# Optimization experiments

Measured on AMD Instinct MI355X. Metric: run time of the kernel, lower is better.

Reference implementation:

```python
import jax, jax.numpy as jnp
import numpy as np

N = 8388608  # batch size
RANGE = 0.02  # self.range in the original module


def setup_inputs() -> dict:
    key = jax.random.key(0)
    k1, k2 = jax.random.split(key)
    preds = jax.random.uniform(k1, (N, 3), dtype=jnp.float32)
    # target is binary ground truth (conditions compare against 0 and 1)
    target = jax.random.randint(k2, (N, 3), 0, 2).astype(jnp.float32)
    return {"preds": preds, "target": target}


def reference(preds, target):
    # Vectorized translation of the per-row scalar branching in RangeLoss.forward.
    p0, p1, p2 = preds[:, 0], preds[:, 1], preds[:, 2]
    t0, t1, t2 = target[:, 0], target[:, 1], target[:, 2]

    # columns 0 and 2: snap target to pred when pred is confidently correct
    t0 = jnp.where((p0 < 0.1) & (t0 == 0.0), p0, t0)
    t0 = jnp.where((p0 > 0.9) & (t0 == 1.0), p0, t0)
    t2 = jnp.where((p2 < 0.1) & (t2 == 0.0), p2, t2)
    t2 = jnp.where((p2 > 0.9) & (t2 == 1.0), p2, t2)

    # column 1: if preds[:,2] > 0.9 take pred; elif pred within +/-RANGE of target take pred
    in_range = (p1 * (1.0 + RANGE) > t1) & (p1 * (1.0 - RANGE) < t1)
    t1 = jnp.where(p2 > 0.9, p1, jnp.where(in_range, p1, t1))

    tgt = jnp.stack([t0, t1, t2], axis=1)  # [N, 3]
    # use_log=False, reduce='mean' in the module defaults
    return jnp.mean((preds - tgt) ** 2)
```

## Files before the change

### kernel.cpp

```cpp
#include <hip/hip_runtime.h>


#define N3      25165824
#define G4      6291456
#define BLOCK   256
#define UNROLL  4
#define NB      (G4 / (BLOCK * UNROLL))
#define INV_TOTAL (1.0f / 25165824.0f)

typedef float vfloat4 __attribute__((ext_vector_type(4)));

__global__ void __launch_bounds__(BLOCK) rangeloss_stage1(
    const vfloat4* __restrict__ preds4,
    const vfloat4* __restrict__ target4,
    const float*   __restrict__ predsf,
    float* __restrict__ partials)
{
    const int base = blockIdx.x * (BLOCK * UNROLL) + threadIdx.x;

    vfloat4 p[UNROLL], t[UNROLL];
    float   pn[UNROLL];

    #pragma unroll
    for (int k = 0; k < UNROLL; ++k) {
        const int i = base + k * BLOCK;
        p[k] = preds4[i];
        t[k] = __builtin_nontemporal_load(&target4[i]);
        pn[k] = predsf[min(4 * i + 4, N3 - 1)];
    }
    __builtin_amdgcn_sched_barrier(0);

    float sum = 0.0f;

    #pragma unroll
    for (int k = 0; k < UNROLL; ++k) {
        const int i  = base + k * BLOCK;
        const int ph = (4 * i) % 3;

        const float pe[4]  = {p[k].x, p[k].y, p[k].z, p[k].w};
        const float te[4]  = {t[k].x, t[k].y, t[k].z, t[k].w};
        const float pnx[4] = {p[k].y, p[k].z, p[k].w, pn[k]};

        #pragma unroll
        for (int e = 0; e < 4; ++e) {
            int col = ph + e;
            col = (col >= 3) ? col - 3 : col;
            const bool is_c1 = (col == 1);

            const float pp = pe[e], tt = te[e];
            const float diff = pp - tt;

            const bool r02 = fabsf(diff) < 0.1f;
            const bool inr = (pp * 1.02f > tt) && (pp * 0.98f < tt);
            const bool r1  = (pnx[e] > 0.9f) || inr;

            const bool snap = is_c1 ? r1 : r02;
            const float d = snap ? 0.0f : diff;
            sum = fmaf(d, d, sum);
        }
    }

    sum *= INV_TOTAL;

    #pragma unroll
    for (int off = 32; off > 0; off >>= 1)
        sum += __shfl_down(sum, off, 64);

    __shared__ float smem[BLOCK / 64];
    const int lane = threadIdx.x & 63;
    const int wave = threadIdx.x >> 6;
    if (lane == 0) smem[wave] = sum;
    __syncthreads();

    if (threadIdx.x == 0)
        partials[blockIdx.x] = smem[0] + smem[1] + smem[2] + smem[3];
}

__global__ void __launch_bounds__(BLOCK) rangeloss_stage2(
    const float* __restrict__ partials,
    float* __restrict__ out)
{
    float sum = 0.0f;
    for (int i = threadIdx.x; i < NB; i += BLOCK)
        sum += partials[i];

    #pragma unroll
    for (int off = 32; off > 0; off >>= 1)
        sum += __shfl_down(sum, off, 64);

    __shared__ float smem[BLOCK / 64];
    const int lane = threadIdx.x & 63;
    const int wave = threadIdx.x >> 6;
    if (lane == 0) smem[wave] = sum;
    __syncthreads();

    if (threadIdx.x == 0)
        out[0] = smem[0] + smem[1] + smem[2] + smem[3];
}

extern "C" void kernel_launch(void* const* d_in, const int* in_sizes, int n_in,
                              void* d_out, int out_size, void* d_ws, size_t ws_size,
                              hipStream_t stream)
{
    const vfloat4* preds4  = (const vfloat4*)d_in[0];
    const vfloat4* target4 = (const vfloat4*)d_in[1];
    const float*   predsf  = (const float*)d_in[0];
    float* partials = (float*)d_ws;
    float* out = (float*)d_out;

    rangeloss_stage1<<<NB, BLOCK, 0, stream>>>(preds4, target4, predsf, partials);
    rangeloss_stage2<<<1, BLOCK, 0, stream>>>(partials, out);
}
```

Measured before the change: 203.5 us.

## Replace strided neighbour-pred load with wave shuffles and halve unroll

Each thread used to issue a scalar gather for the next float after its float4, which is the x lane of its neighbour. That value now comes from a lane shuffle, with wave and block boundaries filled through shared memory and one edge load per block. Unroll drops from 4 to 2 with an occupancy hint, and stage 2 uses a 1024-thread block. In exchange stage 1 gains a block-wide barrier before compute, and the block count doubles.

New measurement: 201.2 us (median of 2 runs). Within noise of the previous version (-1.2%).

```diff
diff --git a/kernel.cpp b/kernel.cpp
--- a/kernel.cpp
+++ b/kernel.cpp
@@ -4,38 +4,62 @@
 #define N3      25165824
 #define G4      6291456
 #define BLOCK   256
-#define UNROLL  4
+#define UNROLL  2
 #define NB      (G4 / (BLOCK * UNROLL))
 #define INV_TOTAL (1.0f / 25165824.0f)
 
 typedef float vfloat4 __attribute__((ext_vector_type(4)));
 
-__global__ void __launch_bounds__(BLOCK) rangeloss_stage1(
+__global__ void __launch_bounds__(BLOCK, 8) rangeloss_stage1(
     const vfloat4* __restrict__ preds4,
     const vfloat4* __restrict__ target4,
     const float*   __restrict__ predsf,
     float* __restrict__ partials)
 {
-    const int base = blockIdx.x * (BLOCK * UNROLL) + threadIdx.x;
+    const int tid  = threadIdx.x;
+    const int lane = tid & 63;
+    const int wv   = tid >> 6;
+    const int base = blockIdx.x * (BLOCK * UNROLL) + tid;
 
     vfloat4 p[UNROLL], t[UNROLL];
-    float   pn[UNROLL];
-
     #pragma unroll
     for (int k = 0; k < UNROLL; ++k) {
         const int i = base + k * BLOCK;
         p[k] = preds4[i];
         t[k] = __builtin_nontemporal_load(&target4[i]);
-        pn[k] = predsf[min(4 * i + 4, N3 - 1)];
+    }
+
+    float edge = 0.0f;
+    if (tid == BLOCK - 1) {
+        const int nf = 4 * (blockIdx.x + 1) * (BLOCK * UNROLL);
+        edge = predsf[min(nf, N3 - 1)];
     }
     __builtin_amdgcn_sched_barrier(0);
 
+    __shared__ float xs[4][UNROLL];
+    if (lane == 0) {
+        #pragma unroll
+        for (int k = 0; k < UNROLL; ++k) xs[wv][k] = p[k].x;
+    }
+    __syncthreads();
+
+    float pn[UNROLL];
+    #pragma unroll
+    for (int k = 0; k < UNROLL; ++k) {
+        float nx = __shfl_down(p[k].x, 1, 64);
+        if (lane == 63) {
+            if (wv < 3)                nx = xs[wv + 1][k];
+            else if (k < UNROLL - 1)   nx = xs[0][k + 1];
+            else                       nx = edge;
+        }
+        pn[k] = nx;
+    }
+
     float sum = 0.0f;
-
     #pragma unroll
     for (int k = 0; k < UNROLL; ++k) {
         const int i  = base + k * BLOCK;
-        const int ph = (4 * i) % 3;
+        const int ph = i % 3;
 
         const float pe[4]  = {p[k].x, p[k].y, p[k].z, p[k].w};
         const float te[4]  = {t[k].x, t[k].y, t[k].z, t[k].w};
@@ -50,7 +74,7 @@
             const float pp = pe[e], tt = te[e];
             const float diff = pp - tt;
 
-            const bool r02 = fabsf(diff) < 0.1f;
+            const bool r02 = __builtin_fabsf(diff) < 0.1f;
             const bool inr = (pp * 1.02f > tt) && (pp * 0.98f < tt);
             const bool r1  = (pnx[e] > 0.9f) || inr;
 
@@ -66,36 +90,41 @@
     for (int off = 32; off > 0; off >>= 1)
         sum += __shfl_down(sum, off, 64);
 
-    __shared__ float smem[BLOCK / 64];
-    const int lane = threadIdx.x & 63;
-    const int wave = threadIdx.x >> 6;
-    if (lane == 0) smem[wave] = sum;
+    __shared__ float red[BLOCK / 64];
+    if (lane == 0) red[wv] = sum;
     __syncthreads();
 
-    if (threadIdx.x == 0)
-        partials[blockIdx.x] = smem[0] + smem[1] + smem[2] + smem[3];
+    if (tid == 0)
+        partials[blockIdx.x] = red[0] + red[1] + red[2] + red[3];
 }
 
-__global__ void __launch_bounds__(BLOCK) rangeloss_stage2(
+#define S2BLOCK 1024
+
+__global__ void __launch_bounds__(S2BLOCK) rangeloss_stage2(
     const float* __restrict__ partials,
     float* __restrict__ out)
 {
     float sum = 0.0f;
-    for (int i = threadIdx.x; i < NB; i += BLOCK)
+    #pragma unroll
+    for (int i = threadIdx.x; i < NB; i += S2BLOCK)
         sum += partials[i];
 
     #pragma unroll
     for (int off = 32; off > 0; off >>= 1)
         sum += __shfl_down(sum, off, 64);
 
-    __shared__ float smem[BLOCK / 64];
+    __shared__ float smem[S2BLOCK / 64];
     const int lane = threadIdx.x & 63;
     const int wave = threadIdx.x >> 6;
     if (lane == 0) smem[wave] = sum;
     __syncthreads();
 
-    if (threadIdx.x == 0)
-        out[0] = smem[0] + smem[1] + smem[2] + smem[3];
+    if (threadIdx.x == 0) {
+        float s = 0.0f;
+        #pragma unroll
+        for (int w = 0; w < S2BLOCK / 64; ++w) s += smem[w];
+        out[0] = s;
+    }
 }
 
 extern "C" void kernel_launch(void* const* d_in, const int* in_sizes, int n_in,
@@ -109,5 +138,5 @@
     float* out = (float*)d_out;
 
     rangeloss_stage1<<<NB, BLOCK, 0, stream>>>(preds4, target4, predsf, partials);
-    rangeloss_stage2<<<1, BLOCK, 0, stream>>>(partials, out);
+    rangeloss_stage2<<<1, S2BLOCK, 0, stream>>>(partials, out);
 }
```
